# Performance work log

Measured on AMD Instinct MI355X. Metric: run time of the kernel, lower is better.

The kernel has to match this reference:

```python
import jax, jax.numpy as jnp
import numpy as np

EMBED_DIM = 1024
NUM_HEADS = 16
HEAD_DIM = EMBED_DIM // NUM_HEADS


def setup_inputs() -> dict:
    key = jax.random.key(0)
    ks = jax.random.split(key, 5)
    B, S, D = 2, 2048, EMBED_DIM
    bound_qkv = 1.0 / np.sqrt(D)
    bound_out = 1.0 / np.sqrt(D)
    return {
        "x": jax.random.normal(ks[0], (B, S, D), dtype=jnp.float32),
        "w_qkv": jax.random.uniform(ks[1], (3 * D, D), jnp.float32, -bound_qkv, bound_qkv),
        "b_qkv": jax.random.uniform(ks[2], (3 * D,), jnp.float32, -bound_qkv, bound_qkv),
        "w_out": jax.random.uniform(ks[3], (D, D), jnp.float32, -bound_out, bound_out),
        "b_out": jax.random.uniform(ks[4], (D,), jnp.float32, -bound_out, bound_out),
    }


def reference(x, w_qkv, b_qkv, w_out, b_out):
    B, S, D = x.shape
    H, Hd = NUM_HEADS, HEAD_DIM
    qkv = x @ w_qkv.T + b_qkv                      # [B,S,3D]
    q, k, v = jnp.split(qkv, 3, axis=-1)           # each [B,S,D]
    # [B,S,D] -> [B,H,S,Hd]
    q = q.reshape(B, S, H, Hd).transpose(0, 2, 1, 3)
    k = k.reshape(B, S, H, Hd).transpose(0, 2, 1, 3)
    v = v.reshape(B, S, H, Hd).transpose(0, 2, 1, 3)
    scores = jnp.einsum("bhqd,bhkd->bhqk", q, k) / np.sqrt(Hd).astype(np.float32)
    probs = jax.nn.softmax(scores, axis=-1)
    attn = jnp.einsum("bhqk,bhkd->bhqd", probs, v)  # [B,H,S,Hd]
    attn = attn.transpose(0, 2, 1, 3).reshape(B, S, D)
    return attn @ w_out.T + b_out
```

## Files before the change

### kernel.cpp

```cpp
#include <hip/hip_runtime.h>

typedef __bf16 bf16_t;
typedef bf16_t bf16x4 __attribute__((ext_vector_type(4)));
typedef bf16_t bf16x8 __attribute__((ext_vector_type(8)));
typedef float f32x4 __attribute__((ext_vector_type(4)));
typedef float f32x16 __attribute__((ext_vector_type(16)));
typedef unsigned short u16;

#define MFMA16(a, b, c) __builtin_amdgcn_mfma_f32_16x16x32_bf16((a), (b), (c), 0, 0, 0)
#define MFMA32(a, b, c) __builtin_amdgcn_mfma_f32_32x32x16_bf16((a), (b), (c), 0, 0, 0)

#define BATCH 2
#define SEQ   2048
#define DIM   1024
#define NH    16
#define HD    64
#define ROWS  (BATCH * SEQ)
#define QKVN  (3 * DIM)
#define GK    1024

__device__ __forceinline__ u16 f2bf(float f) {
    unsigned u = __float_as_uint(f);
    u += 0x7FFFu + ((u >> 16) & 1u);
    return (u16)(u >> 16);
}

__device__ __forceinline__ float exp2_fast(float x) {
    float r;
    asm("v_exp_f32 %0, %1" : "=v"(r) : "v"(x));
    return r;
}

#define PKBF(lo_, hi_) ({ unsigned r_; \
    asm("v_cvt_pk_bf16_f32 %0, %1, %2" : "=v"(r_) : "v"(lo_), "v"(hi_)); r_; })
#define PLSWAP(a_, b_) \
    asm volatile("v_permlane32_swap_b32 %0, %1" : "+v"(a_), "+v"(b_))

#define GLDS(src, dst) __builtin_amdgcn_global_load_lds( \
    (const __attribute__((address_space(1))) void*)(src), \
    (__attribute__((address_space(3))) void*)(dst), 16, 0, 0)

#define WAITB(n) do { \
    asm volatile("s_waitcnt vmcnt(" #n ")" ::: "memory"); \
    __builtin_amdgcn_s_barrier(); } while (0)

__global__ __launch_bounds__(256) void cvt_kernel(
    const float* __restrict__ x,  u16* __restrict__ xb,  int nx4,
    const float* __restrict__ w1, u16* __restrict__ w1b, int n14,
    const float* __restrict__ w2, u16* __restrict__ w2b, int n24)
{
    const int total = nx4 + n14 + n24;
    for (int i = blockIdx.x * 256 + threadIdx.x; i < total; i += gridDim.x * 256) {
        const float4* s; ushort4* d; int o;
        if (i < nx4)             { s = (const float4*)x;  d = (ushort4*)xb;  o = i; }
        else if (i < nx4 + n14)  { s = (const float4*)w1; d = (ushort4*)w1b; o = i - nx4; }
        else                     { s = (const float4*)w2; d = (ushort4*)w2b; o = i - nx4 - n14; }
        float4 v = s[o];
        ushort4 r;
        r.x = f2bf(v.x); r.y = f2bf(v.y); r.z = f2bf(v.z); r.w = f2bf(v.w);
        d[o] = r;
    }
}

__global__ __launch_bounds__(512, 1) void gemm_qkv256(
    const u16* __restrict__ A, const u16* __restrict__ Bt,
    const float* __restrict__ bias, u16* __restrict__ C)
{
    __shared__ u16 As[2][256 * 64];
    __shared__ u16 Bs[2][192 * 64];

    const int tid  = threadIdx.x;
    const int lane = tid & 63;
    const int wave = tid >> 6;
    const int r16  = lane & 15;
    const int grp  = lane >> 4;
    const int wm   = wave >> 2, wn = wave & 3;

    int v = (int)blockIdx.x;
    v = (v & 7) * 32 + (v >> 3);
    const int tm = v >> 4, tn = v & 15;
    const size_t brow = (size_t)tm * 256;
    const size_t bcol = (size_t)tn * 192;

    const int srow = tid >> 3;
    const int aoff = ((tid & 7) ^ (srow & 7)) * 8;
    const u16* pA = A  + (brow + srow) * (size_t)GK + aoff;
    const u16* pB = Bt + (bcol + srow) * (size_t)GK + aoff;

    f32x4 acc[8][3];
    const f32x4 fz = {0.f, 0.f, 0.f, 0.f};
    #pragma unroll
    for (int m = 0; m < 8; ++m)
        #pragma unroll
        for (int n = 0; n < 3; ++n) acc[m][n] = fz;

    const int sw = r16 & 7;
    #define LDA256(buf, mh, mm, ks) \
        (*(const bf16x8*)&(buf)[(wm*128 + (mh)*64 + (mm)*16 + r16)*64 + ((((ks)*4+grp)^sw)*8)])
    #define LDB256(buf, n, ks) \
        (*(const bf16x8*)&(buf)[(wn*48 + (n)*16 + r16)*64 + ((((ks)*4+grp)^sw)*8)])

    {
        u16* Ad = &As[0][(wave * 8) * 64];
        u16* Bd = &Bs[0][(wave * 8) * 64];
        GLDS(pA, Ad);                       GLDS(pA + 64 * GK,  Ad + 64 * 64);
        GLDS(pA + 128 * GK, Ad + 128 * 64); GLDS(pA + 192 * GK, Ad + 192 * 64);
        GLDS(pB, Bd);                       GLDS(pB + 64 * GK,  Bd + 64 * 64);
        GLDS(pB + 128 * GK, Bd + 128 * 64);
    }

    for (int kt = 0; kt < GK / 64; ++kt) {
        const int cur  = kt & 1;
        const bool last = (kt == GK / 64 - 1);
        const int nk = (kt + 1) * 64;
        const u16* Ab = &As[cur][0];
        const u16* Bb = &Bs[cur][0];
        u16* Ad = &As[cur ^ 1][(wave * 8) * 64];
        u16* Bd = &Bs[cur ^ 1][(wave * 8) * 64];
        bf16x8 a[4][2], b0[2][2], b1[2];

        if (!last) {
            GLDS(pA + nk, Ad); GLDS(pA + 64 * GK + nk, Ad + 64 * 64);
            asm volatile("s_waitcnt vmcnt(2)" ::: "memory");
        } else {
            asm volatile("s_waitcnt vmcnt(0)" ::: "memory");
        }
        __builtin_amdgcn_s_barrier();
        #pragma unroll
        for (int mm = 0; mm < 4; ++mm) {
            a[mm][0] = LDA256(Ab, 0, mm, 0); a[mm][1] = LDA256(Ab, 0, mm, 1);
        }
        #pragma unroll
        for (int nn = 0; nn < 2; ++nn) {
            b0[nn][0] = LDB256(Bb, nn, 0); b0[nn][1] = LDB256(Bb, nn, 1);
        }
        __builtin_amdgcn_s_setprio(1);
        #pragma unroll
        for (int mm = 0; mm < 4; ++mm)
            #pragma unroll
            for (int nn = 0; nn < 2; ++nn) {
                acc[mm][nn] = MFMA16(a[mm][0], b0[nn][0], acc[mm][nn]);
                acc[mm][nn] = MFMA16(a[mm][1], b0[nn][1], acc[mm][nn]);
            }
        __builtin_amdgcn_s_setprio(0);
        __builtin_amdgcn_s_barrier();

        if (!last) { GLDS(pA + 128 * GK + nk, Ad + 128 * 64);
                     GLDS(pA + 192 * GK + nk, Ad + 192 * 64); }
        b1[0] = LDB256(Bb, 2, 0); b1[1] = LDB256(Bb, 2, 1);
        __builtin_amdgcn_s_setprio(1);
        #pragma unroll
        for (int mm = 0; mm < 4; ++mm) {
            acc[mm][2] = MFMA16(a[mm][0], b1[0], acc[mm][2]);
            acc[mm][2] = MFMA16(a[mm][1], b1[1], acc[mm][2]);
        }
        __builtin_amdgcn_s_setprio(0);
        __builtin_amdgcn_s_barrier();

        if (!last) { GLDS(pB + nk, Bd); GLDS(pB + 64 * GK + nk, Bd + 64 * 64); }
        #pragma unroll
        for (int mm = 0; mm < 4; ++mm) {
            a[mm][0] = LDA256(Ab, 1, mm, 0); a[mm][1] = LDA256(Ab, 1, mm, 1);
        }
        __builtin_amdgcn_s_setprio(1);
        #pragma unroll
        for (int mm = 0; mm < 4; ++mm) {
            acc[mm + 4][2] = MFMA16(a[mm][0], b1[0], acc[mm + 4][2]);
            acc[mm + 4][2] = MFMA16(a[mm][1], b1[1], acc[mm + 4][2]);
        }
        __builtin_amdgcn_s_setprio(0);
        __builtin_amdgcn_s_barrier();

        if (!last) { GLDS(pB + 128 * GK + nk, Bd + 128 * 64); }
        __builtin_amdgcn_s_setprio(1);
        #pragma unroll
        for (int mm = 0; mm < 4; ++mm)
            #pragma unroll
            for (int nn = 0; nn < 2; ++nn) {
                acc[mm + 4][nn] = MFMA16(a[mm][0], b0[nn][0], acc[mm + 4][nn]);
                acc[mm + 4][nn] = MFMA16(a[mm][1], b0[nn][1], acc[mm + 4][nn]);
            }
        __builtin_amdgcn_s_setprio(0);
        __builtin_amdgcn_s_barrier();
    }

    #pragma unroll
    for (int n = 0; n < 3; ++n) {
        const size_t col = bcol + wn * 48 + n * 16 + r16;
        const float bv = bias[col];
        #pragma unroll
        for (int m = 0; m < 8; ++m) {
            const size_t row0 = brow + wm * 128 + m * 16 + grp * 4;
            if ((int)col >= 2 * DIM) {
                const int c2 = (int)col - 2 * DIM;
                const int d = c2 & 63, h = c2 >> 6;
                const int bb = (int)(row0 >> 11), s0 = (int)(row0 & 2047);
                ushort4 pv;
                pv.x = f2bf(acc[m][n][0] + bv);
                pv.y = f2bf(acc[m][n][1] + bv);
                pv.z = f2bf(acc[m][n][2] + bv);
                pv.w = f2bf(acc[m][n][3] + bv);
                u16* dst = C + ((size_t)bb * 2048 + d * 32 + (s0 >> 6)) * (size_t)QKVN
                             + 2 * DIM + h * 64 + (s0 & 63);
                *(ushort4*)dst = pv;
            } else {
                #pragma unroll
                for (int i = 0; i < 4; ++i)
                    C[(row0 + i) * (size_t)QKVN + col] = f2bf(acc[m][n][i] + bv);
            }
        }
    }
    #undef LDA256
    #undef LDB256
}

__global__ __launch_bounds__(256) void gemm_bt(
    const u16* __restrict__ A, const u16* __restrict__ Bt,
    const float* __restrict__ bias, float* __restrict__ Cv,
    int M, int N, int K)
{
    __shared__ u16 As[128 * 64];
    __shared__ u16 Bs[64 * 64];

    const int tid  = threadIdx.x;
    const int lane = tid & 63;
    const int wave = tid >> 6;
    const int r16  = lane & 15;
    const int grp  = lane >> 4;

    const int nt  = N >> 6;
    const int nwg = (M >> 7) * nt;
    int v = blockIdx.x;
    if ((nwg & 7) == 0) { const int cpx = nwg >> 3; v = (v & 7) * cpx + (v >> 3); }
    const int tm = v / nt, tn = v - tm * nt;
    const size_t brow = (size_t)tm << 7;
    const size_t bcol = (size_t)tn << 6;

    const int wr = wave >> 1, wc = wave & 1;

    f32x4 acc[4][2];
    const f32x4 fz = {0.f, 0.f, 0.f, 0.f};
    #pragma unroll
    for (int m = 0; m < 4; ++m)
        #pragma unroll
        for (int n = 0; n < 2; ++n) acc[m][n] = fz;

    for (int kt = 0; kt < K; kt += 64) {
        #pragma unroll
        for (int it = 0; it < 4; ++it) {
            const int c = it * 256 + tid;
            const u16* ga = A + (brow + (c >> 3)) * (size_t)K + kt + (c & 7) * 8;
            GLDS(ga, &As[(it * 256 + wave * 64) * 8]);
        }
        #pragma unroll
        for (int it = 0; it < 2; ++it) {
            const int c = it * 256 + tid;
            const u16* gb = Bt + (bcol + (c >> 3)) * (size_t)K + kt + (c & 7) * 8;
            GLDS(gb, &Bs[(it * 256 + wave * 64) * 8]);
        }
        __syncthreads();
        #pragma unroll
        for (int ks = 0; ks < 2; ++ks) {
            bf16x8 af[4], bfr[2];
            #pragma unroll
            for (int m = 0; m < 4; ++m)
                af[m] = *(const bf16x8*)&As[(wr * 64 + m * 16 + r16) * 64 + ks * 32 + grp * 8];
            #pragma unroll
            for (int n = 0; n < 2; ++n)
                bfr[n] = *(const bf16x8*)&Bs[(wc * 32 + n * 16 + r16) * 64 + ks * 32 + grp * 8];
            #pragma unroll
            for (int m = 0; m < 4; ++m)
                #pragma unroll
                for (int n = 0; n < 2; ++n)
                    acc[m][n] = MFMA16(af[m], bfr[n], acc[m][n]);
        }
        __syncthreads();
    }

    #pragma unroll
    for (int n = 0; n < 2; ++n) {
        const size_t col = bcol + wc * 32 + n * 16 + r16;
        const float bv = bias[col];
        #pragma unroll
        for (int m = 0; m < 4; ++m) {
            const size_t row0 = brow + wr * 64 + m * 16 + grp * 4;
            #pragma unroll
            for (int i = 0; i < 4; ++i)
                Cv[(row0 + i) * (size_t)N + col] = acc[m][n][i] + bv;
        }
    }
}

__global__ __launch_bounds__(512, 4) void attn_kernel(
    const u16* __restrict__ qkv, u16* __restrict__ attb)
{
    __shared__ u16 smem[8][64 * 64];

    const int tid  = threadIdx.x;
    const int lane = tid & 63;
    const int wave = tid >> 6;
    const int half = wave >> 2;
    const int w4   = wave & 3;
    const int hb   = half * 4;
    const int l31  = lane & 31;
    const int hi   = lane >> 5;
    const int k7   = l31 & 7;

    int v = (int)blockIdx.x;
    v = (v & 7) * 64 + (v >> 3);
    const int bh = v >> 4, qblk = v & 15;
    const int b  = bh >> 4, h = bh & 15;
    const int bS = b * SEQ;
    const int q0w = qblk * 128 + w4 * 32;

    bf16x8 qf[4];
    {
        const u16* qp = qkv + (size_t)(bS + q0w + l31) * QKVN + h * HD + hi * 8;
        #pragma unroll
        for (int m = 0; m < 4; ++m) qf[m] = *(const bf16x8*)(qp + m * 16);
    }

    const f32x16 fz16 = {0,0,0,0,0,0,0,0,0,0,0,0,0,0,0,0};
    f32x16 o0 = fz16, o1 = fz16;
    float lsum = 0.f;

    const int r0 = w4 * 16 + (lane >> 3);
    const int r1 = r0 + 8;
    const u16* kbase = qkv + (size_t)bS * QKVN + DIM + h * HD;
    const char* kp0 = (const char*)(kbase + (size_t)(r0 + half * 1024) * QKVN)
                      + (((lane & 7) * 16) ^ ((r0 & 7) << 4));
    const char* kp1 = (const char*)(kbase + (size_t)(r1 + half * 1024) * QKVN)
                      + (((lane & 7) * 16) ^ ((r1 & 7) << 4));
    const u16* vtb = qkv + (size_t)bS * QKVN + 2 * DIM + h * HD;
    const char* vp0 = (const char*)(vtb + (size_t)(r0 * 32 + half * 16) * QKVN)
                      + (((lane & 7) * 16) ^ ((r0 & 7) << 4));
    const char* vp1 = (const char*)(vtb + (size_t)(r1 * 32 + half * 16) * QKVN)
                      + (((lane & 7) * 16) ^ ((r1 & 7) << 4));

    auto stage = [&](int bsel) {
        u16* kd = &smem[hb + bsel][(w4 * 16) * 64];
        u16* vd = &smem[hb + 2 + bsel][(w4 * 16) * 64];
        GLDS(kp0, kd);
        GLDS(kp1, kd + 8 * 64);
        GLDS(vp0, vd);
        GLDS(vp1, vd + 8 * 64);
        kp0 += 64 * QKVN * 2; kp1 += 64 * QKVN * 2;
        vp0 += QKVN * 2;      vp1 += QKVN * 2;
    };

    const float C1 = 0.125f * 1.44269504f;
    const float C2 = -8.0f * 1.44269504f;

    auto compute_tile = [&](const u16* kb_, const u16* vb_) {
        const char* kc = (const char*)kb_;
        const char* vc = (const char*)vb_;
        bf16x8 paf[4];

        #pragma unroll
        for (int kt = 0; kt < 2; ++kt) {
            bf16x8 kf[4];
            #pragma unroll
            for (int m = 0; m < 4; ++m)
                kf[m] = *(const bf16x8*)(kc + (kt * 32 + l31) * 128
                                            + (((m * 2 + hi) ^ k7) * 16));
            f32x16 s = fz16;
            __builtin_amdgcn_s_setprio(1);
            #pragma unroll
            for (int m = 0; m < 4; ++m) s = MFMA32(kf[m], qf[m], s);
            __builtin_amdgcn_s_setprio(0);

            float p[16];
            #pragma unroll
            for (int r = 0; r < 16; ++r) {
                p[r] = exp2_fast(fmaf(s[r], C1, C2));
                lsum += p[r];
            }
            unsigned A = PKBF(p[0], p[1]),  Bw = PKBF(p[2], p[3]);
            unsigned C = PKBF(p[4], p[5]),  D  = PKBF(p[6], p[7]);
            unsigned E = PKBF(p[8], p[9]),  F  = PKBF(p[10], p[11]);
            unsigned G = PKBF(p[12], p[13]), H = PKBF(p[14], p[15]);
            PLSWAP(A, C); PLSWAP(Bw, D); PLSWAP(E, G); PLSWAP(F, H);
            union { unsigned u[4]; bf16x8 v8; } w0 = {{A, Bw, C, D}},
                                                w1 = {{E, F, G, H}};
            paf[kt * 2]     = w0.v8;
            paf[kt * 2 + 1] = w1.v8;
        }

        __builtin_amdgcn_s_setprio(1);
        #pragma unroll
        for (int m2 = 0; m2 < 4; ++m2) {
            const int cs = ((m2 * 2 + hi) ^ k7) * 16;
            const bf16x8 vf0 = *(const bf16x8*)(vc + l31 * 128 + cs);
            const bf16x8 vf1 = *(const bf16x8*)(vc + (32 + l31) * 128 + cs);
            o0 = MFMA32(paf[m2], vf0, o0);
            o1 = MFMA32(paf[m2], vf1, o1);
        }
        __builtin_amdgcn_s_setprio(0);
    };

    stage(0);
    asm volatile("s_waitcnt vmcnt(0)" ::: "memory");
    __builtin_amdgcn_s_barrier();

    for (int it = 0; it < 8; ++it) {
        stage(1);
        compute_tile(&smem[hb][0], &smem[hb + 2][0]);
        WAITB(0);
        if (it < 7) stage(0);
        compute_tile(&smem[hb + 1][0], &smem[hb + 3][0]);
        WAITB(0);
    }

    float* obuf = (float*)&smem[0][0];
    const int cidx = (w4 * 64 + lane) * 36;
    if (half == 1) {
        #pragma unroll
        for (int r = 0; r < 16; ++r) {
            obuf[cidx + r]      = o0[r];
            obuf[cidx + 16 + r] = o1[r];
        }
        obuf[cidx + 32] = lsum;
    }
    __syncthreads();
    if (half == 0) {
        #pragma unroll
        for (int r = 0; r < 16; ++r) {
            o0[r] += obuf[cidx + r];
            o1[r] += obuf[cidx + 16 + r];
        }
        lsum += obuf[cidx + 32];

        const float ltot = lsum + __shfl_xor(lsum, 32, 64);
        const float rinv = 1.0f / ltot;

        u16* ob = attb + (size_t)(bS + q0w) * DIM + h * HD + l31;
        #pragma unroll
        for (int r = 0; r < 16; ++r) {
            const int q = (r & 3) + 8 * (r >> 2) + 4 * hi;
            const float iv = __shfl(rinv, q, 64);
            u16* pr = ob + (size_t)q * DIM;
            pr[0]  = f2bf(o0[r] * iv);
            pr[32] = f2bf(o1[r] * iv);
        }
    }
}

extern "C" void kernel_launch(void* const* d_in, const int* in_sizes, int n_in,
                              void* d_out, int out_size, void* d_ws, size_t ws_size,
                              hipStream_t stream)
{
    const float* x     = (const float*)d_in[0];
    const float* w_qkv = (const float*)d_in[1];
    const float* b_qkv = (const float*)d_in[2];
    const float* w_out = (const float*)d_in[3];
    const float* b_out = (const float*)d_in[4];
    float* out = (float*)d_out;

    u16* ws   = (u16*)d_ws;
    u16* XB   = ws;
    u16* WQB  = ws + 4194304;
    u16* WOB  = ws + 7340032;
    u16* QKVB = ws + 8388608;
    u16* ATTB = ws + 20971520;

    cvt_kernel<<<2048, 256, 0, stream>>>(x, XB, (ROWS * DIM) / 4,
                                         w_qkv, WQB, (QKVN * DIM) / 4,
                                         w_out, WOB, (DIM * DIM) / 4);

    gemm_qkv256<<<(ROWS / 256) * (QKVN / 192), 512, 0, stream>>>(
        XB, WQB, b_qkv, QKVB);

    attn_kernel<<<BATCH * NH * (SEQ / 128), 512, 0, stream>>>(QKVB, ATTB);

    gemm_bt<<<(ROWS / 128) * (DIM / 64), 256, 0, stream>>>(
        ATTB, WOB, b_out, out, ROWS, DIM, GK);
}
```

Before: 117.0 us.

## Double-buffer out-projection GEMM LDS loads and pack softmax scale FMAs

The output-projection GEMM now uses two LDS buffers and prefetches the next K tile via global_load_lds while the current tile feeds the MFMAs. It waits with a partial vmcnt plus a barrier instead of a full __syncthreads, and raises wave priority around the MFMA block. The attention softmax replaces scalar FMAs with packed v_pk_fma_f32 and moves the row-sum into a separate loop. The goal is to hide global load latency in the GEMM and cut VALU instruction count in attention, at the price of twice the GEMM LDS footprint, which may lower occupancy.

Result: slower. 123.7 us (+5.7%).

```diff
diff --git a/kernel.cpp b/kernel.cpp
--- a/kernel.cpp
+++ b/kernel.cpp
@@ -3,6 +3,7 @@
 typedef __bf16 bf16_t;
 typedef bf16_t bf16x4 __attribute__((ext_vector_type(4)));
 typedef bf16_t bf16x8 __attribute__((ext_vector_type(8)));
+typedef float f32x2 __attribute__((ext_vector_type(2)));
 typedef float f32x4 __attribute__((ext_vector_type(4)));
 typedef float f32x16 __attribute__((ext_vector_type(16)));
 typedef unsigned short u16;
@@ -30,6 +31,9 @@
     asm("v_exp_f32 %0, %1" : "=v"(r) : "v"(x));
     return r;
 }
+
+#define PKFMA(d_, a_, b_, c_) \
+    asm("v_pk_fma_f32 %0, %1, %2, %3" : "=v"(d_) : "v"(a_), "v"(b_), "v"(c_))
 
 #define PKBF(lo_, hi_) ({ unsigned r_; \
     asm("v_cvt_pk_bf16_f32 %0, %1, %2" : "=v"(r_) : "v"(lo_), "v"(hi_)); r_; })
@@ -219,8 +223,8 @@
     const float* __restrict__ bias, float* __restrict__ Cv,
     int M, int N, int K)
 {
-    __shared__ u16 As[128 * 64];
-    __shared__ u16 Bs[64 * 64];
+    __shared__ u16 As[2][128 * 64];
+    __shared__ u16 Bs[2][64 * 64];
 
     const int tid  = threadIdx.x;
     const int lane = tid & 63;
@@ -245,36 +249,52 @@
         #pragma unroll
         for (int n = 0; n < 2; ++n) acc[m][n] = fz;
 
-    for (int kt = 0; kt < K; kt += 64) {
+    auto stage = [&](int buf, int kt) {
         #pragma unroll
         for (int it = 0; it < 4; ++it) {
             const int c = it * 256 + tid;
             const u16* ga = A + (brow + (c >> 3)) * (size_t)K + kt + (c & 7) * 8;
-            GLDS(ga, &As[(it * 256 + wave * 64) * 8]);
+            GLDS(ga, &As[buf][(it * 256 + wave * 64) * 8]);
         }
         #pragma unroll
         for (int it = 0; it < 2; ++it) {
             const int c = it * 256 + tid;
             const u16* gb = Bt + (bcol + (c >> 3)) * (size_t)K + kt + (c & 7) * 8;
-            GLDS(gb, &Bs[(it * 256 + wave * 64) * 8]);
-        }
-        __syncthreads();
+            GLDS(gb, &Bs[buf][(it * 256 + wave * 64) * 8]);
+        }
+    };
+
+    stage(0, 0);
+    const int nkt = K >> 6;
+    for (int kt = 0; kt < nkt; ++kt) {
+        const int buf = kt & 1;
+        if (kt < nkt - 1) {
+            stage(buf ^ 1, (kt + 1) << 6);
+            asm volatile("s_waitcnt vmcnt(6)" ::: "memory");
+        } else {
+            asm volatile("s_waitcnt vmcnt(0)" ::: "memory");
+        }
+        __builtin_amdgcn_s_barrier();
+        const u16* Ab = &As[buf][0];
+        const u16* Bb = &Bs[buf][0];
         #pragma unroll
         for (int ks = 0; ks < 2; ++ks) {
             bf16x8 af[4], bfr[2];
             #pragma unroll
             for (int m = 0; m < 4; ++m)
-                af[m] = *(const bf16x8*)&As[(wr * 64 + m * 16 + r16) * 64 + ks * 32 + grp * 8];
+                af[m] = *(const bf16x8*)&Ab[(wr * 64 + m * 16 + r16) * 64 + ks * 32 + grp * 8];
             #pragma unroll
             for (int n = 0; n < 2; ++n)
-                bfr[n] = *(const bf16x8*)&Bs[(wc * 32 + n * 16 + r16) * 64 + ks * 32 + grp * 8];
+                bfr[n] = *(const bf16x8*)&Bb[(wc * 32 + n * 16 + r16) * 64 + ks * 32 + grp * 8];
+            __builtin_amdgcn_s_setprio(1);
             #pragma unroll
             for (int m = 0; m < 4; ++m)
                 #pragma unroll
                 for (int n = 0; n < 2; ++n)
                     acc[m][n] = MFMA16(af[m], bfr[n], acc[m][n]);
-        }
-        __syncthreads();
+            __builtin_amdgcn_s_setprio(0);
+        }
+        __builtin_amdgcn_s_barrier();
     }
 
     #pragma unroll
@@ -350,6 +370,8 @@
 
     const float C1 = 0.125f * 1.44269504f;
     const float C2 = -8.0f * 1.44269504f;
+    const f32x2 cc1 = {C1, C1};
+    const f32x2 cc2 = {C2, C2};
 
     auto compute_tile = [&](const u16* kb_, const u16* vb_) {
         const char* kc = (const char*)kb_;
@@ -371,10 +393,15 @@
 
             float p[16];
             #pragma unroll
-            for (int r = 0; r < 16; ++r) {
-                p[r] = exp2_fast(fmaf(s[r], C1, C2));
-                lsum += p[r];
+            for (int i2 = 0; i2 < 8; ++i2) {
+                f32x2 sv = {s[2 * i2], s[2 * i2 + 1]};
+                f32x2 r2;
+                PKFMA(r2, sv, cc1, cc2);
+                p[2 * i2]     = exp2_fast(r2[0]);
+                p[2 * i2 + 1] = exp2_fast(r2[1]);
             }
+            #pragma unroll
+            for (int r = 0; r < 16; ++r) lsum += p[r];
             unsigned A = PKBF(p[0], p[1]),  Bw = PKBF(p[2], p[3]);
             unsigned C = PKBF(p[4], p[5]),  D  = PKBF(p[6], p[7]);
             unsigned E = PKBF(p[8], p[9]),  F  = PKBF(p[10], p[11]);
```
